# Kernel optimization log

Measured on AMD Instinct MI355X. Metric: run time of the kernel, lower is better.

Reference implementation:

```python
import jax, jax.numpy as jnp
import numpy as np

LN_EPS = 1e-5
TOP_K = 2


def setup_inputs() -> dict:
    key = jax.random.key(0)
    ks = jax.random.split(key, 6)
    B, S, D, I, E = 4, 1024, 1024, 4096, 8
    return {
        "hidden_states": jax.random.normal(ks[0], (B, S, D), dtype=jnp.float32),
        "attention_mask": jnp.ones((B, S), dtype=jnp.float32),
        "gate_w": jax.random.normal(ks[1], (E, D), dtype=jnp.float32) * 0.02,
        "w1": jax.random.normal(ks[2], (E, D, I), dtype=jnp.float32) * 0.02,
        "b1": jnp.zeros((E, I), dtype=jnp.float32),
        "w2": jax.random.normal(ks[3], (E, I, D), dtype=jnp.float32) * 0.02,
        "b2": jnp.zeros((E, D), dtype=jnp.float32),
        "ln_gamma": jnp.ones((D,), dtype=jnp.float32),
        "ln_beta": jnp.zeros((D,), dtype=jnp.float32),
    }


def reference(hidden_states, attention_mask, gate_w, w1, b1, w2, b2, ln_gamma, ln_beta):
    B, S, D = hidden_states.shape
    E = gate_w.shape[0]
    h = hidden_states.reshape(-1, D).astype(jnp.float32)  # (T, D)

    # --- gate: softmax over experts, top-2, renormalize ---
    logits = h @ gate_w.T                                  # (T, E)
    probs = jax.nn.softmax(logits, axis=-1)
    rw, sel = jax.lax.top_k(probs, TOP_K)                  # (T, k), (T, k)
    rw = rw / jnp.sum(rw, axis=-1, keepdims=True)

    # per-token dense combine weights: (T, E), zero for non-selected experts
    onehot = jax.nn.one_hot(sel, E, dtype=rw.dtype)        # (T, k, E)
    w_te = jnp.einsum('tk,tke->te', rw, onehot)            # (T, E)

    # --- expert FFNs (dense over all experts; weights zero-out non-selected) ---
    mid = jax.nn.gelu(jnp.einsum('td,edi->eti', h, w1) + b1[:, None, :], approximate=False)
    eout = jnp.einsum('eti,eid->etd', mid, w2) + b2[:, None, :]  # (E, T, D)
    moe_out = jnp.einsum('etd,te->td', eout, w_te)         # (T, D)

    out = moe_out.reshape(B, S, D) * attention_mask[..., None]
    out = hidden_states + out

    # LayerNorm
    mu = jnp.mean(out, axis=-1, keepdims=True)
    var = jnp.var(out, axis=-1, keepdims=True)
    out = (out - mu) * jax.lax.rsqrt(var + LN_EPS) * ln_gamma + ln_beta

    # load balancing loss: mse(expert_usage, uniform)
    T = h.shape[0]
    usage = jnp.sum(onehot, axis=(0, 1)) / T               # (E,)
    aux_loss = jnp.mean((usage - 1.0 / E) ** 2)
    return out, aux_loss
```

## Files before the change

kernel.cpp:

```cpp
#include <hip/hip_runtime.h>
#include <hip/hip_bf16.h>
#include <math.h>

#define T_TOK 4096
#define D_DIM 1024
#define I_DIM 4096
#define E_EXP 8
#define MAX_TILES 40

typedef __attribute__((ext_vector_type(8))) short bf16x8;
typedef __attribute__((ext_vector_type(4))) float f32x4;

__device__ __forceinline__ unsigned short f2bf(float x) {
    unsigned int u = __float_as_uint(x);
    u += 0x7fffu + ((u >> 16) & 1u);
    return (unsigned short)(u >> 16);
}

__device__ __forceinline__ void glds16(const unsigned short* g, unsigned short* l) {
    __builtin_amdgcn_global_load_lds(
        (const __attribute__((address_space(1))) unsigned int*)g,
        (__attribute__((address_space(3))) unsigned int*)(unsigned int)(unsigned long long)(void*)l,
        16, 0, 0);
}

#define VMWAIT4 asm volatile("s_waitcnt vmcnt(4)" ::: "memory")
#define VMWAIT0 asm volatile("s_waitcnt vmcnt(0)" ::: "memory")
#define LGKM0   asm volatile("s_waitcnt lgkmcnt(0)" ::: "memory")

__device__ __forceinline__ void bar() {
    __builtin_amdgcn_s_barrier();
}

__global__ void gate_kernel(const float* __restrict__ h, const float* __restrict__ gw,
                            int* __restrict__ counts, int* __restrict__ sel,
                            float* __restrict__ wgt) {
    int t = blockIdx.x;
    int tid = threadIdx.x;
    float acc[E_EXP];
#pragma unroll
    for (int e = 0; e < E_EXP; e++) acc[e] = 0.f;
    const float* hr = h + (size_t)t * D_DIM;
    for (int d = tid; d < D_DIM; d += 256) {
        float hv = hr[d];
#pragma unroll
        for (int e = 0; e < E_EXP; e++) acc[e] += hv * gw[e * D_DIM + d];
    }
#pragma unroll
    for (int e = 0; e < E_EXP; e++)
        for (int off = 32; off > 0; off >>= 1) acc[e] += __shfl_down(acc[e], off, 64);
    __shared__ float red[4][E_EXP];
    int wave = tid >> 6, lane = tid & 63;
    if (lane == 0) {
#pragma unroll
        for (int e = 0; e < E_EXP; e++) red[wave][e] = acc[e];
    }
    __syncthreads();
    if (tid == 0) {
        float lg[E_EXP];
#pragma unroll
        for (int e = 0; e < E_EXP; e++) lg[e] = red[0][e] + red[1][e] + red[2][e] + red[3][e];
        float mx = lg[0];
#pragma unroll
        for (int e = 1; e < E_EXP; e++) mx = fmaxf(mx, lg[e]);
        float p[E_EXP];
#pragma unroll
        for (int e = 0; e < E_EXP; e++) p[e] = expf(lg[e] - mx);
        int i0 = 0; float b0 = p[0];
#pragma unroll
        for (int e = 1; e < E_EXP; e++) if (p[e] > b0) { b0 = p[e]; i0 = e; }
        int i1 = -1; float b1v = -1.f;
#pragma unroll
        for (int e = 0; e < E_EXP; e++) if (e != i0 && p[e] > b1v) { b1v = p[e]; i1 = e; }
        float den = b0 + b1v;
        sel[2 * t] = i0; sel[2 * t + 1] = i1;
        wgt[2 * t] = b0 / den; wgt[2 * t + 1] = b1v / den;
        atomicAdd(&counts[i0], 1);
        atomicAdd(&counts[i1], 1);
    }
}

__global__ void offsets_kernel(const int* __restrict__ counts, int* __restrict__ offs,
                               int* __restrict__ cursors, float* __restrict__ aux_out,
                               int* __restrict__ tile_e, int* __restrict__ tile_m,
                               int* __restrict__ ntiles) {
    if (blockIdx.x == 0 && threadIdx.x == 0) {
        int off = 0; float aux = 0.f; int nt = 0;
        for (int e = 0; e < E_EXP; e++) {
            offs[e] = off; off += counts[e]; cursors[e] = 0;
            float u = (float)counts[e] / (float)T_TOK;
            float d = u - 1.0f / (float)E_EXP;
            aux += d * d;
            for (int m0 = 0; m0 < counts[e]; m0 += 256) {
                tile_e[nt] = e; tile_m[nt] = m0; nt++;
            }
        }
        ntiles[0] = nt;
        aux_out[0] = aux / (float)E_EXP;
    }
}

__global__ void scatter_kernel(const int* __restrict__ sel, const float* __restrict__ wgt,
                               const int* __restrict__ offs, int* __restrict__ cursors,
                               int* __restrict__ tok_list, float* __restrict__ tok_w,
                               int* __restrict__ slot_of) {
    int t = blockIdx.x * 256 + threadIdx.x;
    if (t >= T_TOK) return;
#pragma unroll
    for (int k = 0; k < 2; k++) {
        int e = sel[2 * t + k];
        int pos = atomicAdd(&cursors[e], 1);
        int idx = offs[e] + pos;
        tok_list[idx] = t;
        tok_w[idx] = wgt[2 * t + k];
        slot_of[2 * t + k] = idx;
    }
}

__global__ void cvtH_kernel(const float* __restrict__ src, unsigned short* __restrict__ dst) {
    size_t i = ((size_t)blockIdx.x * 256 + threadIdx.x) * 8;
    float4 a = *(const float4*)(src + i);
    float4 b = *(const float4*)(src + i + 4);
    union { unsigned short u[8]; uint4 v; } o;
    o.u[0] = f2bf(a.x); o.u[1] = f2bf(a.y); o.u[2] = f2bf(a.z); o.u[3] = f2bf(a.w);
    o.u[4] = f2bf(b.x); o.u[5] = f2bf(b.y); o.u[6] = f2bf(b.z); o.u[7] = f2bf(b.w);
    *(uint4*)(dst + i) = o.v;
}

__global__ void transpose_cvt_kernel(const float* __restrict__ src, unsigned short* __restrict__ dst,
                                     int R, int C) {
    __shared__ float tile[32][33];
    int e = blockIdx.z;
    const float* s = src + (size_t)e * R * C;
    unsigned short* d = dst + (size_t)e * R * C;
    int c0 = blockIdx.x * 32, r0 = blockIdx.y * 32;
    int tx = threadIdx.x, ty = threadIdx.y;
#pragma unroll
    for (int j = 0; j < 4; j++)
        tile[ty + 8 * j][tx] = s[(size_t)(r0 + ty + 8 * j) * C + c0 + tx];
    __syncthreads();
#pragma unroll
    for (int j = 0; j < 4; j++)
        d[(size_t)(c0 + ty + 8 * j) * R + r0 + tx] = f2bf(tile[tx][ty + 8 * j]);
}

template <int MODE>
__launch_bounds__(512, 2)
__global__ void moe_gemm_kernel(const unsigned short* __restrict__ Abase,
                                const unsigned short* __restrict__ Bt,
                                const float* __restrict__ bias,
                                const int* __restrict__ counts, const int* __restrict__ offs,
                                const int* __restrict__ tile_e, const int* __restrict__ tile_m,
                                const int* __restrict__ ntiles,
                                const int* __restrict__ tok_list, const float* __restrict__ tok_w,
                                unsigned short* __restrict__ midout, float* __restrict__ slotbuf) {
    constexpr int K  = (MODE == 0) ? D_DIM : I_DIM;
    constexpr int N  = (MODE == 0) ? I_DIM : D_DIM;
    constexpr int NT = K / 32;

    __shared__ __align__(16) unsigned short lA[4][256 * 32];
    __shared__ __align__(16) unsigned short lB[4][256 * 32];

    const int nwg  = gridDim.x * gridDim.y;
    const int flat = blockIdx.y * gridDim.x + blockIdx.x;
    const int q8 = nwg >> 3, r8 = nwg & 7;
    const int xcd = flat & 7, pos = flat >> 3;
    const int id2 = (xcd < r8 ? xcd * (q8 + 1) : r8 * (q8 + 1) + (xcd - r8) * q8) + pos;
    const int tix = id2 / gridDim.y;
    const int nb  = id2 % gridDim.y;
    if (tix >= ntiles[0]) return;

    const int e   = tile_e[tix];
    const int m0  = tile_m[tix];
    const int Ne  = counts[e];
    const int seg = offs[e];
    const int n0  = nb * 256;

    const int tid  = threadIdx.x;
    const int w    = tid >> 6;
    const int lane = tid & 63;
    const int quad = lane >> 4;
    const int l15  = lane & 15;
    const int wm   = (w >> 2) * 128;
    const int wn   = (w & 3) * 64;

    const int lrow = lane >> 2;
    const int scol = (((lane & 3) ^ ((lane >> 3) & 3)) & 3) * 8;
    const int rs   = (((quad ^ ((l15 >> 1) & 3)) & 3) * 8);

    const unsigned short *gA0, *gA1;
    {
        int mr0 = m0 + w * 32 + lrow;
        int mr1 = mr0 + 16;
        int c0 = (mr0 < Ne) ? mr0 : 0;
        int c1 = (mr1 < Ne) ? mr1 : 0;
        size_t r0, r1;
        if (MODE == 0) { r0 = (size_t)tok_list[seg + c0] * K; r1 = (size_t)tok_list[seg + c1] * K; }
        else           { r0 = (size_t)(seg + c0) * K;         r1 = (size_t)(seg + c1) * K; }
        gA0 = Abase + r0 + scol;
        gA1 = Abase + r1 + scol;
    }
    const unsigned short* Bte = Bt + (size_t)e * N * K;
    const unsigned short* gB0 = Bte + (size_t)(n0 + w * 32 + lrow) * K + scol;
    const unsigned short* gB1 = gB0 + (size_t)16 * K;

    auto ISSUE_A = [&](int t) {
        const int b = t & 3, off = t * 32;
        glds16(gA0 + off, &lA[b][w * 1024]);
        glds16(gA1 + off, &lA[b][w * 1024 + 512]);
    };
    auto ISSUE_B = [&](int t) {
        const int b = t & 3, off = t * 32;
        glds16(gB0 + off, &lB[b][w * 1024]);
        glds16(gB1 + off, &lB[b][w * 1024 + 512]);
    };

    f32x4 acc[8][4];
#pragma unroll
    for (int a = 0; a < 8; a++)
#pragma unroll
        for (int j = 0; j < 4; j++) acc[a][j] = (f32x4){0.f, 0.f, 0.f, 0.f};

    bf16x8 bv[4], av[4];
    auto READ_BV = [&](int t) {
        const unsigned short* LB = lB[t & 3];
#pragma unroll
        for (int j = 0; j < 4; j++)
            bv[j] = *(const bf16x8*)&LB[(wn + j * 16 + l15) * 32 + rs];
    };
    auto READ_AV = [&](int t, int pm) {
        const unsigned short* LA = lA[t & 3];
#pragma unroll
        for (int ii = 0; ii < 4; ii++)
            av[ii] = *(const bf16x8*)&LA[(wm + pm * 64 + ii * 16 + l15) * 32 + rs];
    };
    auto MFMA16 = [&](int pm) {
        __builtin_amdgcn_s_setprio(1);
#pragma unroll
        for (int ii = 0; ii < 4; ii++)
#pragma unroll
            for (int j = 0; j < 4; j++)
                acc[pm * 4 + ii][j] = __builtin_amdgcn_mfma_f32_16x16x32_bf16(
                    av[ii], bv[j], acc[pm * 4 + ii][j], 0, 0, 0);
        __builtin_amdgcn_s_setprio(0);
    };

    ISSUE_A(0); ISSUE_B(0);
    ISSUE_A(1); ISSUE_B(1);
    VMWAIT4;
    bar();

    for (int kt = 0; kt < NT - 2; kt += 2) {
        READ_BV(kt); READ_AV(kt, 0);
        ISSUE_A(kt + 2);
        bar(); LGKM0; MFMA16(0); bar();
        READ_AV(kt, 1);
        ISSUE_B(kt + 2);
        VMWAIT4;
        bar(); LGKM0; MFMA16(1); bar();
        READ_BV(kt + 1); READ_AV(kt + 1, 0);
        ISSUE_A(kt + 3);
        bar(); LGKM0; MFMA16(0); bar();
        READ_AV(kt + 1, 1);
        ISSUE_B(kt + 3);
        VMWAIT4;
        bar(); LGKM0; MFMA16(1); bar();
    }
    {
        READ_BV(NT - 2); READ_AV(NT - 2, 0);
        bar(); LGKM0; MFMA16(0); bar();
        READ_AV(NT - 2, 1);
        VMWAIT0;
        bar(); LGKM0; MFMA16(1); bar();
        READ_BV(NT - 1); READ_AV(NT - 1, 0);
        bar(); LGKM0; MFMA16(0); bar();
        READ_AV(NT - 1, 1);
        LGKM0; MFMA16(1);
    }

    const float* be = bias + (size_t)e * N;
#pragma unroll
    for (int a = 0; a < 8; a++) {
        const int mbase = m0 + wm + (a >> 2) * 64 + (a & 3) * 16 + quad * 4;
#pragma unroll
        for (int j = 0; j < 4; j++) {
            const int n = n0 + wn + j * 16 + l15;
            const float bvl = be[n];
#pragma unroll
            for (int r = 0; r < 4; r++) {
                const int m = mbase + r;
                if (m < Ne) {
                    float v = acc[a][j][r] + bvl;
                    if (MODE == 0) {
                        v = 0.5f * v * (1.0f + erff(v * 0.70710678118654752f));
                        midout[(size_t)(seg + m) * N + n] = f2bf(v);
                    } else {
                        slotbuf[(size_t)(seg + m) * N + n] = tok_w[seg + m] * v;
                    }
                }
            }
        }
    }
}

__global__ void ln_kernel(const float* __restrict__ hs, const float* __restrict__ mask,
                          const float* __restrict__ slotbuf, const int* __restrict__ slot_of,
                          const float* __restrict__ gamma, const float* __restrict__ beta,
                          float* __restrict__ outp) {
    int t = blockIdx.x, tid = threadIdx.x;
    int s0 = slot_of[2 * t], s1 = slot_of[2 * t + 1];
    float mk = mask[t];
    const float4* hr = (const float4*)(hs + (size_t)t * D_DIM);
    const float4* p0 = (const float4*)(slotbuf + (size_t)s0 * D_DIM);
    const float4* p1 = (const float4*)(slotbuf + (size_t)s1 * D_DIM);
    float4 hv = hr[tid], a = p0[tid], b = p1[tid];
    float x0 = hv.x + mk * (a.x + b.x);
    float x1 = hv.y + mk * (a.y + b.y);
    float x2 = hv.z + mk * (a.z + b.z);
    float x3 = hv.w + mk * (a.w + b.w);
    float sum = x0 + x1 + x2 + x3;
    float sq = x0 * x0 + x1 * x1 + x2 * x2 + x3 * x3;
    for (int off = 32; off > 0; off >>= 1) {
        sum += __shfl_down(sum, off, 64);
        sq += __shfl_down(sq, off, 64);
    }
    __shared__ float rsum[4], rsq[4];
    __shared__ float mu_s, rstd_s;
    int wave = tid >> 6, lane = tid & 63;
    if (lane == 0) { rsum[wave] = sum; rsq[wave] = sq; }
    __syncthreads();
    if (tid == 0) {
        float s = rsum[0] + rsum[1] + rsum[2] + rsum[3];
        float q = rsq[0] + rsq[1] + rsq[2] + rsq[3];
        float mu = s / (float)D_DIM;
        float var = q / (float)D_DIM - mu * mu;
        mu_s = mu; rstd_s = rsqrtf(var + 1e-5f);
    }
    __syncthreads();
    float mu = mu_s, rstd = rstd_s;
    const float4* g4 = (const float4*)gamma;
    const float4* b4 = (const float4*)beta;
    float4 g = g4[tid], bb = b4[tid];
    float4 o;
    o.x = (x0 - mu) * rstd * g.x + bb.x;
    o.y = (x1 - mu) * rstd * g.y + bb.y;
    o.z = (x2 - mu) * rstd * g.z + bb.z;
    o.w = (x3 - mu) * rstd * g.w + bb.w;
    ((float4*)(outp + (size_t)t * D_DIM))[tid] = o;
}

extern "C" void kernel_launch(void* const* d_in, const int* in_sizes, int n_in,
                              void* d_out, int out_size, void* d_ws, size_t ws_size,
                              hipStream_t stream) {
    const float* hs    = (const float*)d_in[0];
    const float* mask  = (const float*)d_in[1];
    const float* gw    = (const float*)d_in[2];
    const float* w1    = (const float*)d_in[3];
    const float* b1    = (const float*)d_in[4];
    const float* w2    = (const float*)d_in[5];
    const float* b2    = (const float*)d_in[6];
    const float* gamma = (const float*)d_in[7];
    const float* beta  = (const float*)d_in[8];
    float* out = (float*)d_out;

    char* ws = (char*)d_ws;
    int*   counts   = (int*)(ws + 0);
    int*   cursors  = (int*)(ws + 64);
    int*   offs     = (int*)(ws + 128);
    int*   ntiles   = (int*)(ws + 256);
    int*   tile_e   = (int*)(ws + 512);
    int*   tile_m   = (int*)(ws + 1024);
    int*   sel      = (int*)(ws + 4096);
    float* wgt      = (float*)(ws + 4096 + 1 * 32768);
    int*   slot_of  = (int*)(ws + 4096 + 2 * 32768);
    int*   tok_list = (int*)(ws + 4096 + 3 * 32768);
    float* tok_w    = (float*)(ws + 4096 + 4 * 32768);
    unsigned short* Hbf = (unsigned short*)(ws + (1ull << 20));
    unsigned short* W1t = (unsigned short*)(ws + (9ull << 20));
    unsigned short* W2t = (unsigned short*)(ws + (73ull << 20));
    unsigned short* mid = (unsigned short*)(ws + (137ull << 20));
    float* slotbuf      = (float*)(ws + (201ull << 20));

    hipMemsetAsync(counts, 0, 64, stream);
    gate_kernel<<<T_TOK, 256, 0, stream>>>(hs, gw, counts, sel, wgt);
    offsets_kernel<<<1, 64, 0, stream>>>(counts, offs, cursors, out + (size_t)T_TOK * D_DIM,
                                         tile_e, tile_m, ntiles);
    scatter_kernel<<<T_TOK / 256, 256, 0, stream>>>(sel, wgt, offs, cursors, tok_list, tok_w, slot_of);
    cvtH_kernel<<<(T_TOK * D_DIM / 8) / 256, 256, 0, stream>>>(hs, Hbf);
    transpose_cvt_kernel<<<dim3(I_DIM / 32, D_DIM / 32, E_EXP), dim3(32, 8), 0, stream>>>(w1, W1t, D_DIM, I_DIM);
    transpose_cvt_kernel<<<dim3(D_DIM / 32, I_DIM / 32, E_EXP), dim3(32, 8), 0, stream>>>(w2, W2t, I_DIM, D_DIM);
    moe_gemm_kernel<0><<<dim3(MAX_TILES, I_DIM / 256), 512, 0, stream>>>(
        Hbf, W1t, b1, counts, offs, tile_e, tile_m, ntiles, tok_list, tok_w, mid, nullptr);
    moe_gemm_kernel<1><<<dim3(MAX_TILES, D_DIM / 256), 512, 0, stream>>>(
        mid, W2t, b2, counts, offs, tile_e, tile_m, ntiles, tok_list, tok_w, nullptr, slotbuf);
    ln_kernel<<<T_TOK, 256, 0, stream>>>(hs, mask, slotbuf, slot_of, gamma, beta, out);
}
```

Baseline: 777.2 us.

## Shrink MoE GEMM tiles to 128x128 with simpler double-buffered pipeline

```diff
diff --git a/kernel.cpp b/kernel.cpp
--- a/kernel.cpp
+++ b/kernel.cpp
@@ -6,7 +6,7 @@
 #define D_DIM 1024
 #define I_DIM 4096
 #define E_EXP 8
-#define MAX_TILES 40
+#define MAX_TILES 72
 
 typedef __attribute__((ext_vector_type(8))) short bf16x8;
 typedef __attribute__((ext_vector_type(4))) float f32x4;
@@ -26,10 +26,11 @@
 
 #define VMWAIT4 asm volatile("s_waitcnt vmcnt(4)" ::: "memory")
 #define VMWAIT0 asm volatile("s_waitcnt vmcnt(0)" ::: "memory")
-#define LGKM0   asm volatile("s_waitcnt lgkmcnt(0)" ::: "memory")
 
 __device__ __forceinline__ void bar() {
+    asm volatile("" ::: "memory");
     __builtin_amdgcn_s_barrier();
+    asm volatile("" ::: "memory");
 }
 
 __global__ void gate_kernel(const float* __restrict__ h, const float* __restrict__ gw,
@@ -91,7 +92,7 @@
             float u = (float)counts[e] / (float)T_TOK;
             float d = u - 1.0f / (float)E_EXP;
             aux += d * d;
-            for (int m0 = 0; m0 < counts[e]; m0 += 256) {
+            for (int m0 = 0; m0 < counts[e]; m0 += 128) {
                 tile_e[nt] = e; tile_m[nt] = m0; nt++;
             }
         }
@@ -145,7 +146,7 @@
 }
 
 template <int MODE>
-__launch_bounds__(512, 2)
+__launch_bounds__(256, 4)
 __global__ void moe_gemm_kernel(const unsigned short* __restrict__ Abase,
                                 const unsigned short* __restrict__ Bt,
                                 const float* __restrict__ bias,
@@ -158,8 +159,8 @@
     constexpr int N  = (MODE == 0) ? I_DIM : D_DIM;
     constexpr int NT = K / 32;
 
-    __shared__ __align__(16) unsigned short lA[4][256 * 32];
-    __shared__ __align__(16) unsigned short lB[4][256 * 32];
+    __shared__ __align__(16) unsigned short lA[2][128 * 32];
+    __shared__ __align__(16) unsigned short lB[2][128 * 32];
 
     const int nwg  = gridDim.x * gridDim.y;
     const int flat = blockIdx.y * gridDim.x + blockIdx.x;
@@ -174,15 +175,15 @@
     const int m0  = tile_m[tix];
     const int Ne  = counts[e];
     const int seg = offs[e];
-    const int n0  = nb * 256;
+    const int n0  = nb * 128;
 
     const int tid  = threadIdx.x;
     const int w    = tid >> 6;
     const int lane = tid & 63;
     const int quad = lane >> 4;
     const int l15  = lane & 15;
-    const int wm   = (w >> 2) * 128;
-    const int wn   = (w & 3) * 64;
+    const int wm   = (w >> 1) * 64;
+    const int wn   = (w & 1) * 64;
 
     const int lrow = lane >> 2;
     const int scol = (((lane & 3) ^ ((lane >> 3) & 3)) & 3) * 8;
@@ -204,84 +205,52 @@
     const unsigned short* gB0 = Bte + (size_t)(n0 + w * 32 + lrow) * K + scol;
     const unsigned short* gB1 = gB0 + (size_t)16 * K;
 
-    auto ISSUE_A = [&](int t) {
-        const int b = t & 3, off = t * 32;
-        glds16(gA0 + off, &lA[b][w * 1024]);
-        glds16(gA1 + off, &lA[b][w * 1024 + 512]);
+    auto STAGE = [&](int t) {
+        const int b = t & 1, off = t * 32;
+        glds16(gA0 + off, &lA[b][(w * 32) * 32]);
+        glds16(gA1 + off, &lA[b][(w * 32 + 16) * 32]);
+        glds16(gB0 + off, &lB[b][(w * 32) * 32]);
+        glds16(gB1 + off, &lB[b][(w * 32 + 16) * 32]);
     };
-    auto ISSUE_B = [&](int t) {
-        const int b = t & 3, off = t * 32;
-        glds16(gB0 + off, &lB[b][w * 1024]);
-        glds16(gB1 + off, &lB[b][w * 1024 + 512]);
-    };
-
-    f32x4 acc[8][4];
-#pragma unroll
-    for (int a = 0; a < 8; a++)
-#pragma unroll
-        for (int j = 0; j < 4; j++) acc[a][j] = (f32x4){0.f, 0.f, 0.f, 0.f};
-
-    bf16x8 bv[4], av[4];
-    auto READ_BV = [&](int t) {
-        const unsigned short* LB = lB[t & 3];
+
+    f32x4 acc[4][4];
+#pragma unroll
+    for (int i = 0; i < 4; i++)
+#pragma unroll
+        for (int j = 0; j < 4; j++) acc[i][j] = (f32x4){0.f, 0.f, 0.f, 0.f};
+
+    STAGE(0);
+    for (int kt = 0; kt < NT; ++kt) {
+        if (kt + 1 < NT) {
+            STAGE(kt + 1);
+            VMWAIT4;
+        } else {
+            VMWAIT0;
+        }
+        bar();
+        const unsigned short* LA = lA[kt & 1];
+        const unsigned short* LB = lB[kt & 1];
+        bf16x8 av[4], bv[4];
+#pragma unroll
+        for (int i = 0; i < 4; i++)
+            av[i] = *(const bf16x8*)&LA[(wm + i * 16 + l15) * 32 + rs];
 #pragma unroll
         for (int j = 0; j < 4; j++)
             bv[j] = *(const bf16x8*)&LB[(wn + j * 16 + l15) * 32 + rs];
-    };
-    auto READ_AV = [&](int t, int pm) {
-        const unsigned short* LA = lA[t & 3];
-#pragma unroll
-        for (int ii = 0; ii < 4; ii++)
-            av[ii] = *(const bf16x8*)&LA[(wm + pm * 64 + ii * 16 + l15) * 32 + rs];
-    };
-    auto MFMA16 = [&](int pm) {
         __builtin_amdgcn_s_setprio(1);
 #pragma unroll
-        for (int ii = 0; ii < 4; ii++)
+        for (int i = 0; i < 4; i++)
 #pragma unroll
             for (int j = 0; j < 4; j++)
-                acc[pm * 4 + ii][j] = __builtin_amdgcn_mfma_f32_16x16x32_bf16(
-                    av[ii], bv[j], acc[pm * 4 + ii][j], 0, 0, 0);
+                acc[i][j] = __builtin_amdgcn_mfma_f32_16x16x32_bf16(av[i], bv[j], acc[i][j], 0, 0, 0);
         __builtin_amdgcn_s_setprio(0);
-    };
-
-    ISSUE_A(0); ISSUE_B(0);
-    ISSUE_A(1); ISSUE_B(1);
-    VMWAIT4;
-    bar();
-
-    for (int kt = 0; kt < NT - 2; kt += 2) {
-        READ_BV(kt); READ_AV(kt, 0);
-        ISSUE_A(kt + 2);
-        bar(); LGKM0; MFMA16(0); bar();
-        READ_AV(kt, 1);
-        ISSUE_B(kt + 2);
-        VMWAIT4;
-        bar(); LGKM0; MFMA16(1); bar();
-        READ_BV(kt + 1); READ_AV(kt + 1, 0);
-        ISSUE_A(kt + 3);
-        bar(); LGKM0; MFMA16(0); bar();
-        READ_AV(kt + 1, 1);
-        ISSUE_B(kt + 3);
-        VMWAIT4;
-        bar(); LGKM0; MFMA16(1); bar();
-    }
-    {
-        READ_BV(NT - 2); READ_AV(NT - 2, 0);
-        bar(); LGKM0; MFMA16(0); bar();
-        READ_AV(NT - 2, 1);
-        VMWAIT0;
-        bar(); LGKM0; MFMA16(1); bar();
-        READ_BV(NT - 1); READ_AV(NT - 1, 0);
-        bar(); LGKM0; MFMA16(0); bar();
-        READ_AV(NT - 1, 1);
-        LGKM0; MFMA16(1);
+        bar();
     }
 
     const float* be = bias + (size_t)e * N;
 #pragma unroll
-    for (int a = 0; a < 8; a++) {
-        const int mbase = m0 + wm + (a >> 2) * 64 + (a & 3) * 16 + quad * 4;
+    for (int i = 0; i < 4; i++) {
+        const int mbase = m0 + wm + i * 16 + quad * 4;
 #pragma unroll
         for (int j = 0; j < 4; j++) {
             const int n = n0 + wn + j * 16 + l15;
@@ -290,7 +259,7 @@
             for (int r = 0; r < 4; r++) {
                 const int m = mbase + r;
                 if (m < Ne) {
-                    float v = acc[a][j][r] + bvl;
+                    float v = acc[i][j][r] + bvl;
                     if (MODE == 0) {
                         v = 0.5f * v * (1.0f + erff(v * 0.70710678118654752f));
                         midout[(size_t)(seg + m) * N + n] = f2bf(v);
@@ -389,9 +358,9 @@
     cvtH_kernel<<<(T_TOK * D_DIM / 8) / 256, 256, 0, stream>>>(hs, Hbf);
     transpose_cvt_kernel<<<dim3(I_DIM / 32, D_DIM / 32, E_EXP), dim3(32, 8), 0, stream>>>(w1, W1t, D_DIM, I_DIM);
     transpose_cvt_kernel<<<dim3(D_DIM / 32, I_DIM / 32, E_EXP), dim3(32, 8), 0, stream>>>(w2, W2t, I_DIM, D_DIM);
-    moe_gemm_kernel<0><<<dim3(MAX_TILES, I_DIM / 256), 512, 0, stream>>>(
+    moe_gemm_kernel<0><<<dim3(MAX_TILES, I_DIM / 128), 256, 0, stream>>>(
         Hbf, W1t, b1, counts, offs, tile_e, tile_m, ntiles, tok_list, tok_w, mid, nullptr);
-    moe_gemm_kernel<1><<<dim3(MAX_TILES, D_DIM / 256), 512, 0, stream>>>(
+    moe_gemm_kernel<1><<<dim3(MAX_TILES, D_DIM / 128), 256, 0, stream>>>(
         mid, W2t, b2, counts, offs, tile_e, tile_m, ntiles, tok_list, tok_w, nullptr, slotbuf);
     ln_kernel<<<T_TOK, 256, 0, stream>>>(hs, mask, slotbuf, slot_of, gamma, beta, out);
 }
```

Measured after the change: 734.6 us. -5.5%, faster.
